# Performance work log

Hardware: AMD Instinct MI355X
Metric: run time of the kernel (lower is better)

The kernel has to match this reference:

```python
import jax, jax.numpy as jnp
import numpy as np

NUM_STREAM = 4
SINKHORN_ITERS = 20
HC_EPS = 1e-06
NORM_EPS = 1e-06


def sinkhorn_knopps(h, iters, eps):
    # h: [B, S, ns, ns]
    h = jax.nn.softmax(h, axis=-1) + eps
    h = h / (h.sum(-2, keepdims=True) + eps)
    for _ in range(iters - 1):  # fixed small trip count (19), unrolled
        h = h / (h.sum(-1, keepdims=True) + eps)
        h = h / (h.sum(-2, keepdims=True) + eps)
    return h


def setup_inputs() -> dict:
    key = jax.random.key(0)
    k1, k2, k3, k4 = jax.random.split(key, 4)
    B, S, ns, H = 4, 2048, NUM_STREAM, 1024
    mix_hc = (2 + ns) * ns  # 24
    x = jax.random.normal(k1, (B, S, ns, H), dtype=jnp.float32)
    hc_fn = jax.random.normal(k2, (mix_hc, ns * H), dtype=jnp.float32) * 0.02
    hc_scale = jax.random.uniform(k3, (3,), dtype=jnp.float32)
    hc_base = jax.random.normal(k4, (mix_hc,), dtype=jnp.float32)
    return {"x": x, "hc_fn": hc_fn, "hc_scale": hc_scale, "hc_base": hc_base}


def reference(x, hc_fn, hc_scale, hc_base):
    B, S, ns, H = x.shape
    xf = x.reshape(B, S, ns * H).astype(jnp.float32)
    # RMSNorm stats (applied as a post-scale on the linear output, as in source)
    rsqrt = jax.lax.rsqrt(jnp.mean(jnp.square(xf), axis=-1, keepdims=True) + NORM_EPS)
    weight = jnp.einsum('bsd,md->bsm', xf, hc_fn) * rsqrt  # [B, S, mix_hc]
    h_pre = weight[..., :ns]
    h_post = weight[..., ns:2 * ns]
    h_res = weight[..., 2 * ns:].reshape(B, S, ns, ns)
    h_pre = jax.nn.sigmoid(h_pre * hc_scale[0] + hc_base[:ns][None, None, :]) + HC_EPS
    h_post = 2.0 * jax.nn.sigmoid(h_post * hc_scale[1] + hc_base[ns:2 * ns][None, None, :])
    h_res = h_res * hc_scale[2] + hc_base[2 * ns:].reshape(ns, ns)[None, None, :, :]
    h_res = sinkhorn_knopps(h_res, SINKHORN_ITERS, HC_EPS)
    xs = xf.reshape(B, S, ns, H)
    # hc_pre: mix streams into a single vector per token
    y = jnp.einsum('bsn,bsnh->bsh', h_pre, xs)  # [B, S, H]
    # hc_post: broadcast gated y back to streams + Sinkhorn-mixed residual streams
    out = h_post[..., None] * y[:, :, None, :] + jnp.einsum('bsij,bsih->bsjh', h_res, xs)
    return out.astype(x.dtype)
```

## Files before the change

kernel.cpp:

```cpp
#include <hip/hip_runtime.h>
#include <math.h>

#define NS 4
#define HDIM 1024
#define DDIM 4096
#define T 4
#define NTH 512
#define HC_EPS_F 1e-6f
#define NORM_EPS_F 1e-6f

__device__ __forceinline__ float frcp(float v) { return __builtin_amdgcn_rcpf(v); }

__device__ __forceinline__ void gload_lds16(const float* g, float* l) {
  __builtin_amdgcn_global_load_lds(
      (const __attribute__((address_space(1))) void*)g,
      (__attribute__((address_space(3))) void*)l, 16, 0, 0);
}

__launch_bounds__(NTH, 2)
__global__ void mhc_onepass(const float* __restrict__ x,
                            const float* __restrict__ hc_fn,
                            const float* __restrict__ hc_scale,
                            const float* __restrict__ hc_base,
                            float* __restrict__ out) {
  __shared__ float xs[T * DDIM];
  __shared__ float w_s[25][T];
  __shared__ float g_s[24][T];

  const int tid  = threadIdx.x;
  const int lane = tid & 63;
  const int wave = tid >> 6;
  const long long tok0 = (long long)blockIdx.x * T;
  const float* xg = x + tok0 * DDIM;

  #pragma unroll
  for (int c = 0; c < 8; ++c)
    gload_lds16(xg + (c * NTH + tid) * 4, xs + (size_t)(c * NTH + wave * 64) * 4);

  const int mb = wave * 3;
  const float4* fn4[3];
  #pragma unroll
  for (int m = 0; m < 3; ++m)
    fn4[m] = (const float4*)(hc_fn + (long long)(mb + m) * DDIM);

  float acc[3][T];
  #pragma unroll
  for (int m = 0; m < 3; ++m)
    #pragma unroll
    for (int t = 0; t < T; ++t) acc[m][t] = 0.f;
  float ssq = 0.f;

  float4 c_fn[3];
  #pragma unroll
  for (int m = 0; m < 3; ++m) c_fn[m] = fn4[m][lane];

  __syncthreads();

  const float4* xs4 = (const float4*)xs;
  #pragma unroll 2
  for (int it = 0; it < 16; ++it) {
    float4 n_fn[3];
    if (it < 15) {
      const int nfl = (it + 1) * 64 + lane;
      #pragma unroll
      for (int m = 0; m < 3; ++m) n_fn[m] = fn4[m][nfl];
    }
    const int fl = it * 64 + lane;
    const float4 xv0 = xs4[fl];
    const float4 xv1 = xs4[1024 + fl];
    const float4 xv2 = xs4[2048 + fl];
    const float4 xv3 = xs4[3072 + fl];

    if (wave < 4) {
      const float4 xw = (wave == 0) ? xv0 : (wave == 1) ? xv1 : (wave == 2) ? xv2 : xv3;
      ssq = fmaf(xw.x, xw.x, fmaf(xw.y, xw.y, fmaf(xw.z, xw.z, fmaf(xw.w, xw.w, ssq))));
    }
    #pragma unroll
    for (int m = 0; m < 3; ++m) {
      acc[m][0] = fmaf(xv0.x, c_fn[m].x, fmaf(xv0.y, c_fn[m].y,
                  fmaf(xv0.z, c_fn[m].z, fmaf(xv0.w, c_fn[m].w, acc[m][0]))));
      acc[m][1] = fmaf(xv1.x, c_fn[m].x, fmaf(xv1.y, c_fn[m].y,
                  fmaf(xv1.z, c_fn[m].z, fmaf(xv1.w, c_fn[m].w, acc[m][1]))));
      acc[m][2] = fmaf(xv2.x, c_fn[m].x, fmaf(xv2.y, c_fn[m].y,
                  fmaf(xv2.z, c_fn[m].z, fmaf(xv2.w, c_fn[m].w, acc[m][2]))));
      acc[m][3] = fmaf(xv3.x, c_fn[m].x, fmaf(xv3.y, c_fn[m].y,
                  fmaf(xv3.z, c_fn[m].z, fmaf(xv3.w, c_fn[m].w, acc[m][3]))));
    }
    if (it < 15) {
      #pragma unroll
      for (int m = 0; m < 3; ++m) c_fn[m] = n_fn[m];
    }
  }

  #pragma unroll
  for (int m = 0; m < 3; ++m)
    #pragma unroll
    for (int t = 0; t < T; ++t) {
      float v = acc[m][t];
      #pragma unroll
      for (int off = 32; off > 0; off >>= 1) v += __shfl_xor(v, off, 64);
      if (lane == 0) w_s[mb + m][t] = v;
    }
  if (wave < 4) {
    float v = ssq;
    #pragma unroll
    for (int off = 32; off > 0; off >>= 1) v += __shfl_xor(v, off, 64);
    if (lane == 0) w_s[24][wave] = v;
  }
  __syncthreads();

  if (wave == 0) {
    const int tt = lane >> 4;
    const int e  = lane & 15;
    const float rs = rsqrtf(w_s[24][tt] * (1.0f / DDIM) + NORM_EPS_F);
    const float s0 = hc_scale[0], s1 = hc_scale[1], s2 = hc_scale[2];

    float h = w_s[8 + e][tt] * rs * s2 + hc_base[8 + e];
    float mx = fmaxf(h, __shfl_xor(h, 1, 4));
    mx = fmaxf(mx, __shfl_xor(mx, 2, 4));
    float ex = expf(h - mx);
    float sm = ex + __shfl_xor(ex, 1, 4);
    sm += __shfl_xor(sm, 2, 4);
    h = ex * frcp(sm) + HC_EPS_F;
    float cs = h + __shfl_xor(h, 4, 16);
    cs += __shfl_xor(cs, 8, 16);
    h *= frcp(cs + HC_EPS_F);
    #pragma unroll 1
    for (int itn = 0; itn < 19; ++itn) {
      float rsum = h + __shfl_xor(h, 1, 4);
      rsum += __shfl_xor(rsum, 2, 4);
      h *= frcp(rsum + HC_EPS_F);
      float csum = h + __shfl_xor(h, 4, 16);
      csum += __shfl_xor(csum, 8, 16);
      h *= frcp(csum + HC_EPS_F);
    }
    g_s[8 + e][tt] = h;
    if (e < NS) {
      const float wp = w_s[e][tt] * rs;
      g_s[e][tt] = frcp(1.0f + expf(-(wp * s0 + hc_base[e]))) + HC_EPS_F;
      const float wq = w_s[NS + e][tt] * rs;
      g_s[NS + e][tt] = 2.0f * frcp(1.0f + expf(-(wq * s1 + hc_base[NS + e])));
    }
  }
  __syncthreads();

  {
    const int tt   = wave >> 1;
    const int half = wave & 1;
    float hp[NS], hq[NS], hr[NS][NS];
    #pragma unroll
    for (int i = 0; i < NS; ++i) {
      hp[i] = g_s[i][tt];
      hq[i] = g_s[NS + i][tt];
      #pragma unroll
      for (int j = 0; j < NS; ++j) hr[i][j] = g_s[8 + i * NS + j][tt];
    }
    float4* ob = (float4*)(out + (tok0 + tt) * DDIM);
    #pragma unroll
    for (int c = 0; c < 2; ++c) {
      const int h4 = half * 128 + c * 64 + lane;
      float4 xv[NS];
      #pragma unroll
      for (int i = 0; i < NS; ++i) xv[i] = xs4[tt * 1024 + i * 256 + h4];
      float4 y;
      y.x = hp[0]*xv[0].x + hp[1]*xv[1].x + hp[2]*xv[2].x + hp[3]*xv[3].x;
      y.y = hp[0]*xv[0].y + hp[1]*xv[1].y + hp[2]*xv[2].y + hp[3]*xv[3].y;
      y.z = hp[0]*xv[0].z + hp[1]*xv[1].z + hp[2]*xv[2].z + hp[3]*xv[3].z;
      y.w = hp[0]*xv[0].w + hp[1]*xv[1].w + hp[2]*xv[2].w + hp[3]*xv[3].w;
      #pragma unroll
      for (int n = 0; n < NS; ++n) {
        float4 o;
        o.x = hq[n]*y.x + hr[0][n]*xv[0].x + hr[1][n]*xv[1].x + hr[2][n]*xv[2].x + hr[3][n]*xv[3].x;
        o.y = hq[n]*y.y + hr[0][n]*xv[0].y + hr[1][n]*xv[1].y + hr[2][n]*xv[2].y + hr[3][n]*xv[3].y;
        o.z = hq[n]*y.z + hr[0][n]*xv[0].z + hr[1][n]*xv[1].z + hr[2][n]*xv[2].z + hr[3][n]*xv[3].z;
        o.w = hq[n]*y.w + hr[0][n]*xv[0].w + hr[1][n]*xv[1].w + hr[2][n]*xv[2].w + hr[3][n]*xv[3].w;
        ob[n * 256 + h4] = o;
      }
    }
  }
}

extern "C" void kernel_launch(void* const* d_in, const int* in_sizes, int n_in,
                              void* d_out, int out_size, void* d_ws, size_t ws_size,
                              hipStream_t stream) {
  const float* x        = (const float*)d_in[0];
  const float* hc_fn    = (const float*)d_in[1];
  const float* hc_scale = (const float*)d_in[2];
  const float* hc_base  = (const float*)d_in[3];
  float* out = (float*)d_out;

  const int ntok = in_sizes[0] / DDIM;
  mhc_onepass<<<ntok / T, NTH, 0, stream>>>(x, hc_fn, hc_scale, hc_base, out);
}
```

Measured before the change: 99.89 us.

## Process eight token groups per block with double-buffered LDS prefetch

Each block now loops over eight groups of four tokens instead of handling a single group. The next group's x tile is loaded into a second LDS buffer with async global-to-LDS loads while the current group is computed, aiming to hide global load latency behind the projection, Sinkhorn and output stages. The grid shrinks eightfold and LDS use per block doubles to about 128KB, so likely only one block fits per CU. That lowers occupancy, and the serial single-wave Sinkhorn step stays on the critical path of every group.

```diff
diff --git a/kernel.cpp b/kernel.cpp
--- a/kernel.cpp
+++ b/kernel.cpp
@@ -5,6 +5,7 @@
 #define HDIM 1024
 #define DDIM 4096
 #define T 4
+#define GRP 8
 #define NTH 512
 #define HC_EPS_F 1e-6f
 #define NORM_EPS_F 1e-6f
@@ -16,6 +17,14 @@
       (const __attribute__((address_space(1))) void*)g,
       (__attribute__((address_space(3))) void*)l, 16, 0, 0);
 }
+
+#define SOFT_BARRIER()                                          \
+  do {                                                          \
+    asm volatile("s_waitcnt lgkmcnt(0)" ::: "memory");          \
+    __builtin_amdgcn_sched_barrier(0);                          \
+    __builtin_amdgcn_s_barrier();                               \
+    __builtin_amdgcn_sched_barrier(0);                          \
+  } while (0)
 
 __launch_bounds__(NTH, 2)
 __global__ void mhc_onepass(const float* __restrict__ x,
@@ -23,19 +32,14 @@
                             const float* __restrict__ hc_scale,
                             const float* __restrict__ hc_base,
                             float* __restrict__ out) {
-  __shared__ float xs[T * DDIM];
+  __shared__ float xs[2][T * DDIM];
   __shared__ float w_s[25][T];
   __shared__ float g_s[24][T];
 
   const int tid  = threadIdx.x;
   const int lane = tid & 63;
   const int wave = tid >> 6;
-  const long long tok0 = (long long)blockIdx.x * T;
-  const float* xg = x + tok0 * DDIM;
-
-  #pragma unroll
-  for (int c = 0; c < 8; ++c)
-    gload_lds16(xg + (c * NTH + tid) * 4, xs + (size_t)(c * NTH + wave * 64) * 4);
+  const long long btok0 = (long long)blockIdx.x * (T * GRP);
 
   const int mb = wave * 3;
   const float4* fn4[3];
@@ -43,140 +47,163 @@
   for (int m = 0; m < 3; ++m)
     fn4[m] = (const float4*)(hc_fn + (long long)(mb + m) * DDIM);
 
-  float acc[3][T];
-  #pragma unroll
-  for (int m = 0; m < 3; ++m)
-    #pragma unroll
-    for (int t = 0; t < T; ++t) acc[m][t] = 0.f;
-  float ssq = 0.f;
-
-  float4 c_fn[3];
-  #pragma unroll
-  for (int m = 0; m < 3; ++m) c_fn[m] = fn4[m][lane];
-
-  __syncthreads();
-
-  const float4* xs4 = (const float4*)xs;
-  #pragma unroll 2
-  for (int it = 0; it < 16; ++it) {
-    float4 n_fn[3];
-    if (it < 15) {
-      const int nfl = (it + 1) * 64 + lane;
-      #pragma unroll
-      for (int m = 0; m < 3; ++m) n_fn[m] = fn4[m][nfl];
-    }
-    const int fl = it * 64 + lane;
-    const float4 xv0 = xs4[fl];
-    const float4 xv1 = xs4[1024 + fl];
-    const float4 xv2 = xs4[2048 + fl];
-    const float4 xv3 = xs4[3072 + fl];
-
-    if (wave < 4) {
-      const float4 xw = (wave == 0) ? xv0 : (wave == 1) ? xv1 : (wave == 2) ? xv2 : xv3;
-      ssq = fmaf(xw.x, xw.x, fmaf(xw.y, xw.y, fmaf(xw.z, xw.z, fmaf(xw.w, xw.w, ssq))));
-    }
-    #pragma unroll
-    for (int m = 0; m < 3; ++m) {
-      acc[m][0] = fmaf(xv0.x, c_fn[m].x, fmaf(xv0.y, c_fn[m].y,
-                  fmaf(xv0.z, c_fn[m].z, fmaf(xv0.w, c_fn[m].w, acc[m][0]))));
-      acc[m][1] = fmaf(xv1.x, c_fn[m].x, fmaf(xv1.y, c_fn[m].y,
-                  fmaf(xv1.z, c_fn[m].z, fmaf(xv1.w, c_fn[m].w, acc[m][1]))));
-      acc[m][2] = fmaf(xv2.x, c_fn[m].x, fmaf(xv2.y, c_fn[m].y,
-                  fmaf(xv2.z, c_fn[m].z, fmaf(xv2.w, c_fn[m].w, acc[m][2]))));
-      acc[m][3] = fmaf(xv3.x, c_fn[m].x, fmaf(xv3.y, c_fn[m].y,
-                  fmaf(xv3.z, c_fn[m].z, fmaf(xv3.w, c_fn[m].w, acc[m][3]))));
-    }
-    if (it < 15) {
-      #pragma unroll
-      for (int m = 0; m < 3; ++m) c_fn[m] = n_fn[m];
-    }
-  }
-
-  #pragma unroll
-  for (int m = 0; m < 3; ++m)
-    #pragma unroll
-    for (int t = 0; t < T; ++t) {
-      float v = acc[m][t];
-      #pragma unroll
-      for (int off = 32; off > 0; off >>= 1) v += __shfl_xor(v, off, 64);
-      if (lane == 0) w_s[mb + m][t] = v;
-    }
-  if (wave < 4) {
-    float v = ssq;
-    #pragma unroll
-    for (int off = 32; off > 0; off >>= 1) v += __shfl_xor(v, off, 64);
-    if (lane == 0) w_s[24][wave] = v;
+  const float s0 = hc_scale[0], s1 = hc_scale[1], s2 = hc_scale[2];
+
+  {
+    const float* xg = x + btok0 * DDIM;
+    #pragma unroll
+    for (int c = 0; c < 8; ++c)
+      gload_lds16(xg + (size_t)(c * NTH + tid) * 4,
+                  xs[0] + (size_t)(c * NTH + wave * 64) * 4);
   }
   __syncthreads();
 
-  if (wave == 0) {
-    const int tt = lane >> 4;
-    const int e  = lane & 15;
-    const float rs = rsqrtf(w_s[24][tt] * (1.0f / DDIM) + NORM_EPS_F);
-    const float s0 = hc_scale[0], s1 = hc_scale[1], s2 = hc_scale[2];
-
-    float h = w_s[8 + e][tt] * rs * s2 + hc_base[8 + e];
-    float mx = fmaxf(h, __shfl_xor(h, 1, 4));
-    mx = fmaxf(mx, __shfl_xor(mx, 2, 4));
-    float ex = expf(h - mx);
-    float sm = ex + __shfl_xor(ex, 1, 4);
-    sm += __shfl_xor(sm, 2, 4);
-    h = ex * frcp(sm) + HC_EPS_F;
-    float cs = h + __shfl_xor(h, 4, 16);
-    cs += __shfl_xor(cs, 8, 16);
-    h *= frcp(cs + HC_EPS_F);
-    #pragma unroll 1
-    for (int itn = 0; itn < 19; ++itn) {
-      float rsum = h + __shfl_xor(h, 1, 4);
-      rsum += __shfl_xor(rsum, 2, 4);
-      h *= frcp(rsum + HC_EPS_F);
-      float csum = h + __shfl_xor(h, 4, 16);
-      csum += __shfl_xor(csum, 8, 16);
-      h *= frcp(csum + HC_EPS_F);
-    }
-    g_s[8 + e][tt] = h;
-    if (e < NS) {
-      const float wp = w_s[e][tt] * rs;
-      g_s[e][tt] = frcp(1.0f + expf(-(wp * s0 + hc_base[e]))) + HC_EPS_F;
-      const float wq = w_s[NS + e][tt] * rs;
-      g_s[NS + e][tt] = 2.0f * frcp(1.0f + expf(-(wq * s1 + hc_base[NS + e])));
-    }
-  }
-  __syncthreads();
-
-  {
-    const int tt   = wave >> 1;
-    const int half = wave & 1;
-    float hp[NS], hq[NS], hr[NS][NS];
-    #pragma unroll
-    for (int i = 0; i < NS; ++i) {
-      hp[i] = g_s[i][tt];
-      hq[i] = g_s[NS + i][tt];
-      #pragma unroll
-      for (int j = 0; j < NS; ++j) hr[i][j] = g_s[8 + i * NS + j][tt];
-    }
-    float4* ob = (float4*)(out + (tok0 + tt) * DDIM);
-    #pragma unroll
-    for (int c = 0; c < 2; ++c) {
-      const int h4 = half * 128 + c * 64 + lane;
-      float4 xv[NS];
-      #pragma unroll
-      for (int i = 0; i < NS; ++i) xv[i] = xs4[tt * 1024 + i * 256 + h4];
-      float4 y;
-      y.x = hp[0]*xv[0].x + hp[1]*xv[1].x + hp[2]*xv[2].x + hp[3]*xv[3].x;
-      y.y = hp[0]*xv[0].y + hp[1]*xv[1].y + hp[2]*xv[2].y + hp[3]*xv[3].y;
-      y.z = hp[0]*xv[0].z + hp[1]*xv[1].z + hp[2]*xv[2].z + hp[3]*xv[3].z;
-      y.w = hp[0]*xv[0].w + hp[1]*xv[1].w + hp[2]*xv[2].w + hp[3]*xv[3].w;
-      #pragma unroll
-      for (int n = 0; n < NS; ++n) {
-        float4 o;
-        o.x = hq[n]*y.x + hr[0][n]*xv[0].x + hr[1][n]*xv[1].x + hr[2][n]*xv[2].x + hr[3][n]*xv[3].x;
-        o.y = hq[n]*y.y + hr[0][n]*xv[0].y + hr[1][n]*xv[1].y + hr[2][n]*xv[2].y + hr[3][n]*xv[3].y;
-        o.z = hq[n]*y.z + hr[0][n]*xv[0].z + hr[1][n]*xv[1].z + hr[2][n]*xv[2].z + hr[3][n]*xv[3].z;
-        o.w = hq[n]*y.w + hr[0][n]*xv[0].w + hr[1][n]*xv[1].w + hr[2][n]*xv[2].w + hr[3][n]*xv[3].w;
-        ob[n * 256 + h4] = o;
-      }
-    }
+  for (int g = 0; g < GRP; ++g) {
+    const int cb = g & 1;
+    const long long tok0 = btok0 + (long long)g * T;
+
+    if (g < GRP - 1) {
+      const float* xg = x + (tok0 + T) * DDIM;
+      #pragma unroll
+      for (int c = 0; c < 8; ++c)
+        gload_lds16(xg + (size_t)(c * NTH + tid) * 4,
+                    xs[cb ^ 1] + (size_t)(c * NTH + wave * 64) * 4);
+    }
+
+    float acc[3][T];
+    #pragma unroll
+    for (int m = 0; m < 3; ++m)
+      #pragma unroll
+      for (int t = 0; t < T; ++t) acc[m][t] = 0.f;
+    float ssq = 0.f;
+
+    float4 c_fn[3];
+    #pragma unroll
+    for (int m = 0; m < 3; ++m) c_fn[m] = fn4[m][lane];
+
+    const float4* xs4 = (const float4*)xs[cb];
+    #pragma unroll 2
+    for (int it = 0; it < 16; ++it) {
+      float4 n_fn[3];
+      if (it < 15) {
+        const int nfl = (it + 1) * 64 + lane;
+        #pragma unroll
+        for (int m = 0; m < 3; ++m) n_fn[m] = fn4[m][nfl];
+      }
+      const int fl = it * 64 + lane;
+      const float4 xv0 = xs4[fl];
+      const float4 xv1 = xs4[1024 + fl];
+      const float4 xv2 = xs4[2048 + fl];
+      const float4 xv3 = xs4[3072 + fl];
+
+      if (wave < 4) {
+        const float4 xw = (wave == 0) ? xv0 : (wave == 1) ? xv1 : (wave == 2) ? xv2 : xv3;
+        ssq = fmaf(xw.x, xw.x, fmaf(xw.y, xw.y, fmaf(xw.z, xw.z, fmaf(xw.w, xw.w, ssq))));
+      }
+      #pragma unroll
+      for (int m = 0; m < 3; ++m) {
+        acc[m][0] = fmaf(xv0.x, c_fn[m].x, fmaf(xv0.y, c_fn[m].y,
+                    fmaf(xv0.z, c_fn[m].z, fmaf(xv0.w, c_fn[m].w, acc[m][0]))));
+        acc[m][1] = fmaf(xv1.x, c_fn[m].x, fmaf(xv1.y, c_fn[m].y,
+                    fmaf(xv1.z, c_fn[m].z, fmaf(xv1.w, c_fn[m].w, acc[m][1]))));
+        acc[m][2] = fmaf(xv2.x, c_fn[m].x, fmaf(xv2.y, c_fn[m].y,
+                    fmaf(xv2.z, c_fn[m].z, fmaf(xv2.w, c_fn[m].w, acc[m][2]))));
+        acc[m][3] = fmaf(xv3.x, c_fn[m].x, fmaf(xv3.y, c_fn[m].y,
+                    fmaf(xv3.z, c_fn[m].z, fmaf(xv3.w, c_fn[m].w, acc[m][3]))));
+      }
+      if (it < 15) {
+        #pragma unroll
+        for (int m = 0; m < 3; ++m) c_fn[m] = n_fn[m];
+      }
+    }
+
+    #pragma unroll
+    for (int m = 0; m < 3; ++m)
+      #pragma unroll
+      for (int t = 0; t < T; ++t) {
+        float v = acc[m][t];
+        #pragma unroll
+        for (int off = 32; off > 0; off >>= 1) v += __shfl_xor(v, off, 64);
+        if (lane == 0) w_s[mb + m][t] = v;
+      }
+    if (wave < 4) {
+      float v = ssq;
+      #pragma unroll
+      for (int off = 32; off > 0; off >>= 1) v += __shfl_xor(v, off, 64);
+      if (lane == 0) w_s[24][wave] = v;
+    }
+    SOFT_BARRIER();
+
+    if (wave == 0) {
+      const int tt = lane >> 4;
+      const int e  = lane & 15;
+      const float rs = rsqrtf(w_s[24][tt] * (1.0f / DDIM) + NORM_EPS_F);
+
+      float h = w_s[8 + e][tt] * rs * s2 + hc_base[8 + e];
+      float mx = fmaxf(h, __shfl_xor(h, 1, 4));
+      mx = fmaxf(mx, __shfl_xor(mx, 2, 4));
+      float ex = expf(h - mx);
+      float sm = ex + __shfl_xor(ex, 1, 4);
+      sm += __shfl_xor(sm, 2, 4);
+      h = ex * frcp(sm) + HC_EPS_F;
+      float cs = h + __shfl_xor(h, 4, 16);
+      cs += __shfl_xor(cs, 8, 16);
+      h *= frcp(cs + HC_EPS_F);
+      #pragma unroll 1
+      for (int itn = 0; itn < 19; ++itn) {
+        float rsum = h + __shfl_xor(h, 1, 4);
+        rsum += __shfl_xor(rsum, 2, 4);
+        h *= frcp(rsum + HC_EPS_F);
+        float csum = h + __shfl_xor(h, 4, 16);
+        csum += __shfl_xor(csum, 8, 16);
+        h *= frcp(csum + HC_EPS_F);
+      }
+      g_s[8 + e][tt] = h;
+      if (e < NS) {
+        const float wp = w_s[e][tt] * rs;
+        g_s[e][tt] = frcp(1.0f + expf(-(wp * s0 + hc_base[e]))) + HC_EPS_F;
+        const float wq = w_s[NS + e][tt] * rs;
+        g_s[NS + e][tt] = 2.0f * frcp(1.0f + expf(-(wq * s1 + hc_base[NS + e])));
+      }
+    }
+    SOFT_BARRIER();
+
+    {
+      const int tt   = wave >> 1;
+      const int half = wave & 1;
+      float hp[NS], hq[NS], hr[NS][NS];
+      #pragma unroll
+      for (int i = 0; i < NS; ++i) {
+        hp[i] = g_s[i][tt];
+        hq[i] = g_s[NS + i][tt];
+        #pragma unroll
+        for (int j = 0; j < NS; ++j) hr[i][j] = g_s[8 + i * NS + j][tt];
+      }
+      float4* ob = (float4*)(out + (tok0 + tt) * DDIM);
+      #pragma unroll
+      for (int c = 0; c < 2; ++c) {
+        const int h4 = half * 128 + c * 64 + lane;
+        float4 xv[NS];
+        #pragma unroll
+        for (int i = 0; i < NS; ++i) xv[i] = xs4[tt * 1024 + i * 256 + h4];
+        float4 y;
+        y.x = hp[0]*xv[0].x + hp[1]*xv[1].x + hp[2]*xv[2].x + hp[3]*xv[3].x;
+        y.y = hp[0]*xv[0].y + hp[1]*xv[1].y + hp[2]*xv[2].y + hp[3]*xv[3].y;
+        y.z = hp[0]*xv[0].z + hp[1]*xv[1].z + hp[2]*xv[2].z + hp[3]*xv[3].z;
+        y.w = hp[0]*xv[0].w + hp[1]*xv[1].w + hp[2]*xv[2].w + hp[3]*xv[3].w;
+        #pragma unroll
+        for (int n = 0; n < NS; ++n) {
+          float4 o;
+          o.x = hq[n]*y.x + hr[0][n]*xv[0].x + hr[1][n]*xv[1].x + hr[2][n]*xv[2].x + hr[3][n]*xv[3].x;
+          o.y = hq[n]*y.y + hr[0][n]*xv[0].y + hr[1][n]*xv[1].y + hr[2][n]*xv[2].y + hr[3][n]*xv[3].y;
+          o.z = hq[n]*y.z + hr[0][n]*xv[0].z + hr[1][n]*xv[1].z + hr[2][n]*xv[2].z + hr[3][n]*xv[3].z;
+          o.w = hq[n]*y.w + hr[0][n]*xv[0].w + hr[1][n]*xv[1].w + hr[2][n]*xv[2].w + hr[3][n]*xv[3].w;
+          ob[n * 256 + h4] = o;
+        }
+      }
+    }
+
+    __syncthreads();
   }
 }
 
@@ -190,5 +217,6 @@
   float* out = (float*)d_out;
 
   const int ntok = in_sizes[0] / DDIM;
-  mhc_onepass<<<ntok / T, NTH, 0, stream>>>(x, hc_fn, hc_scale, hc_base, out);
+  const int grid = ntok / (T * GRP);
+  mhc_onepass<<<grid, NTH, 0, stream>>>(x, hc_fn, hc_scale, hc_base, out);
 }
```

Result: slower. 141.3 us (+41.4%).
